# Optimization experiments

Measured on AMD Instinct MI355X. Metric: run time of the kernel, lower is better.

Reference implementation:

```python
import jax, jax.numpy as jnp
import numpy as np

B, T, D = 4, 2048, 1024
EPS = 1e-5


def _layernorm(x, g, b):
    mu = jnp.mean(x, axis=-1, keepdims=True)
    var = jnp.var(x, axis=-1, keepdims=True)
    return (x - mu) * jax.lax.rsqrt(var + EPS) * g + b


def setup_inputs() -> dict:
    key = jax.random.key(0)
    ks = jax.random.split(key, 16)
    s = lambda fan_in: 1.0 / np.sqrt(fan_in)
    return {
        "x": jax.random.normal(ks[0], (B, T, D), dtype=jnp.float32),
        "ln1_g": jnp.ones((D,), jnp.float32),
        "ln1_b": jnp.zeros((D,), jnp.float32),
        "Wqkv": jax.random.uniform(ks[1], (D, 3 * D), jnp.float32, -s(D), s(D)),
        "bqkv": jnp.zeros((3 * D,), jnp.float32),
        "Wproj": jax.random.uniform(ks[2], (D, D), jnp.float32, -s(D), s(D)),
        "bproj": jnp.zeros((D,), jnp.float32),
        "ln2_g": jnp.ones((D,), jnp.float32),
        "ln2_b": jnp.zeros((D,), jnp.float32),
        "W1": jax.random.uniform(ks[3], (D, 4 * D), jnp.float32, -s(D), s(D)),
        "b1": jnp.zeros((4 * D,), jnp.float32),
        "W2": jax.random.uniform(ks[4], (4 * D, D), jnp.float32, -s(4 * D), s(4 * D)),
        "b2": jnp.zeros((D,), jnp.float32),
    }


def reference(x, ln1_g, ln1_b, Wqkv, bqkv, Wproj, bproj, ln2_g, ln2_b, W1, b1, W2, b2):
    # NOTE: no residual connections in the original Block.
    h = _layernorm(x, ln1_g, ln1_b)
    kqv = h @ Wqkv + bqkv                      # [B,T,3D]
    k, q, v = jnp.split(kqv, 3, axis=-1)       # split order: k, q, v
    # Original scales by 1/sqrt(k.size(-1)) AFTER transposing k -> 1/sqrt(T).
    scores = jnp.einsum("btd,bsd->bts", q, k) * (1.0 / np.sqrt(T))
    causal = jnp.tril(jnp.ones((T, T), dtype=bool))
    scores = jnp.where(causal, scores, -jnp.inf)
    attn = jax.nn.softmax(scores, axis=-1)
    a = jnp.einsum("bts,bsd->btd", attn, v)
    a = a @ Wproj + bproj
    h2 = _layernorm(a, ln2_g, ln2_b)
    m = jax.nn.gelu(h2 @ W1 + b1, approximate=True)
    return m @ W2 + b2
```

## Files before the change

kernel.cpp:

```cpp
#include <hip/hip_runtime.h>
#include <hip/hip_bf16.h>

typedef __hip_bfloat16 bf16;
typedef __bf16 bf16x8 __attribute__((ext_vector_type(8)));
typedef __bf16 bf16x4 __attribute__((ext_vector_type(4)));
typedef __bf16 bf16x2 __attribute__((ext_vector_type(2)));
typedef float f32x4 __attribute__((ext_vector_type(4)));

static constexpr int Bq = 4, Tq = 2048, Dq = 1024;

__device__ inline float b2f(bf16 h) { return __bfloat162float(h); }
__device__ inline bf16 f2b(float f) { return __float2bfloat16(f); }

__device__ __forceinline__ void gload_lds16(const bf16* g, bf16* lds_wave_base) {
    __builtin_amdgcn_global_load_lds((const __attribute__((address_space(1))) void*)g,
                                     (__attribute__((address_space(3))) void*)lds_wave_base,
                                     16, 0, 0);
}

__device__ __forceinline__ float fast_gelu(float x) {
    float u = x * (0.7978845608028654f + 0.03567740814183427f * x * x);
    float e = __builtin_amdgcn_exp2f(-2.885390081777927f * u);
    return x * __builtin_amdgcn_rcpf(1.f + e);
}

__device__ inline void ld4f(const float* p, float* v) {
    float4 t = *reinterpret_cast<const float4*>(p);
    v[0] = t.x; v[1] = t.y; v[2] = t.z; v[3] = t.w;
}
__device__ inline void ld4f(const bf16* p, float* v) {
    bf16x4 t = *reinterpret_cast<const bf16x4*>(p);
    v[0] = (float)t[0]; v[1] = (float)t[1]; v[2] = (float)t[2]; v[3] = (float)t[3];
}

template <typename Tin>
__device__ __forceinline__ void ln_body(const Tin* __restrict__ x, const float* __restrict__ g,
                                        const float* __restrict__ b, bf16* __restrict__ out,
                                        int row, float* sred)
{
    const int tid = threadIdx.x;
    const int s0 = tid * 4;
    const Tin* xr = x + (size_t)row * Dq;
    bf16* orow = out + (size_t)row * Dq;
    float v[4], gv[4], bv[4];
    ld4f(xr + s0, v);
    ld4f(g + s0, gv);
    ld4f(b + s0, bv);
    float sum = v[0] + v[1] + v[2] + v[3];
    float sq = v[0]*v[0] + v[1]*v[1] + v[2]*v[2] + v[3]*v[3];
    for (int o = 32; o > 0; o >>= 1) { sum += __shfl_xor(sum, o); sq += __shfl_xor(sq, o); }
    const int w = tid >> 6;
    if ((tid & 63) == 0) { sred[w] = sum; sred[4 + w] = sq; }
    __syncthreads();
    const float ts = sred[0] + sred[1] + sred[2] + sred[3];
    const float tq = sred[4] + sred[5] + sred[6] + sred[7];
    const float mean = ts / Dq;
    const float rs = rsqrtf(tq / Dq - mean * mean + 1e-5f);
    bf16x4 o4;
    #pragma unroll
    for (int i = 0; i < 4; ++i) o4[i] = (__bf16)((v[i] - mean) * rs * gv[i] + bv[i]);
    *reinterpret_cast<bf16x4*>(orow + s0) = o4;
}

__global__ void ln_kernel(const bf16* __restrict__ x, const float* __restrict__ g,
                          const float* __restrict__ b, bf16* __restrict__ out)
{
    __shared__ float sred[8];
    ln_body(x, g, b, out, blockIdx.x, sred);
}

__global__ void prep_kernel(const float* __restrict__ x, const float* __restrict__ g,
                            const float* __restrict__ b, bf16* __restrict__ h,
                            const float* __restrict__ Wqkv, bf16* __restrict__ WqkvT,
                            const float* __restrict__ Wproj, bf16* __restrict__ WprojT,
                            const float* __restrict__ W1, bf16* __restrict__ W1T,
                            const float* __restrict__ W2, bf16* __restrict__ W2T)
{
    __shared__ float smem[64 * 65];
    int id = blockIdx.x;
    if (id < 8192) { ln_body(x, g, b, h, id, smem); return; }
    id -= 8192;
    const float* src; bf16* dst; long ldin, ldout; int gx;
    if (id < 768)       { src = Wqkv;  dst = WqkvT;  ldin = 3072; ldout = 1024; gx = 48; }
    else if (id < 1024) { id -= 768;  src = Wproj; dst = WprojT; ldin = 1024; ldout = 1024; gx = 16; }
    else if (id < 2048) { id -= 1024; src = W1;    dst = W1T;    ldin = 4096; ldout = 1024; gx = 64; }
    else                { id -= 2048; src = W2;    dst = W2T;    ldin = 1024; ldout = 4096; gx = 16; }
    const int c0 = (id % gx) * 64, r0 = (id / gx) * 64;
    const int tid = threadIdx.x;
    const int tx = tid & 63, ty = tid >> 6;
    float (*tile)[65] = reinterpret_cast<float(*)[65]>(smem);
    #pragma unroll
    for (int i = 0; i < 16; ++i) {
        int r = ty + i * 4;
        tile[r][tx] = src[(size_t)(r0 + r) * ldin + c0 + tx];
    }
    __syncthreads();
    const int px = tid & 31, cy = tid >> 5;
    #pragma unroll
    for (int i = 0; i < 8; ++i) {
        int cc = cy + i * 8;
        bf16x2 p;
        p[0] = (__bf16)tile[px * 2][cc];
        p[1] = (__bf16)tile[px * 2 + 1][cc];
        *reinterpret_cast<bf16x2*>(&dst[(size_t)(c0 + cc) * ldout + r0 + px * 2]) = p;
    }
}

__global__ void transpose_b2b_kernel(const bf16* __restrict__ in, bf16* __restrict__ out,
                                     long ldin, long ldout, long inBatch, long outBatch)
{
    __shared__ bf16 tile[64][66];
    const bf16* ip = in + (size_t)blockIdx.z * inBatch;
    bf16* op = out + (size_t)blockIdx.z * outBatch;
    const int c0 = blockIdx.x * 64, r0 = blockIdx.y * 64;
    const int tid = threadIdx.x;
    const int tx = tid & 31, ty = tid >> 5;
    #pragma unroll
    for (int i = 0; i < 8; ++i) {
        int r = ty + i * 8;
        *reinterpret_cast<bf16x2*>(&tile[r][tx * 2]) =
            *reinterpret_cast<const bf16x2*>(&ip[(size_t)(r0 + r) * ldin + c0 + tx * 2]);
    }
    __syncthreads();
    #pragma unroll
    for (int i = 0; i < 8; ++i) {
        int cc = ty + i * 8;
        bf16x2 p;
        p[0] = tile[tx * 2][cc];
        p[1] = tile[tx * 2 + 1][cc];
        *reinterpret_cast<bf16x2*>(&op[(size_t)(c0 + cc) * ldout + r0 + tx * 2]) = p;
    }
}

template <int ACT, int TRI, int CK, int FR>
__global__ void gemm128(const bf16* __restrict__ A, const bf16* __restrict__ Bt,
                        const float* __restrict__ bias,
                        bf16* __restrict__ Cb, float* __restrict__ Cf,
                        int K, long lda, long ldb, long ldc,
                        long sA, long sB, long sC, float scale)
{
    int bx, by;
    if (TRI) {
        const int lin = blockIdx.x;
        int t = (int)((sqrtf(8.f * lin + 1.f) - 1.f) * 0.5f);
        while ((t + 1) * (t + 2) / 2 <= lin) ++t;
        while (t * (t + 1) / 2 > lin) --t;
        by = t; bx = lin - t * (t + 1) / 2;
    } else {
        const int gx = gridDim.x, gy = gridDim.y;
        const int lin = blockIdx.x + gx * blockIdx.y;
        const int band = lin & 7;
        const int idx = lin >> 3;
        bx = idx % gx;
        by = band * (gy >> 3) + idx / gx;
    }

    const int m0 = by * 128, n0 = bx * 128;
    const int Kend = CK ? min(K, m0 + 128) : K;

    __shared__ bf16 As[128 * 64];
    __shared__ bf16 Bs[128 * 64];

    const bf16* Ab = A + (size_t)blockIdx.z * sA;
    const bf16* Bb = Bt + (size_t)blockIdx.z * sB;
    const int tid = threadIdx.x;
    const int wid = tid >> 6, lane = tid & 63;
    const int wr = wid >> 1, wc = wid & 1;
    const int l15 = lane & 15, quad = lane >> 4;

    const int rloc = lane >> 3, slot = lane & 7;
    const bf16* agp = Ab + (size_t)(m0 + wid * 32 + rloc) * lda + (slot ^ rloc) * 8;
    const bf16* bgp = Bb + (size_t)(n0 + wid * 32 + rloc) * ldb + (slot ^ rloc) * 8;
    bf16* awb = As + wid * 32 * 64;
    bf16* bwb = Bs + wid * 32 * 64;

    const int afo = (wr * 64 + l15) * 64 + ((quad ^ (l15 & 7)) * 8);
    const int bfo = (wc * 64 + l15) * 64 + ((quad ^ (l15 & 7)) * 8);

    f32x4 acc[4][4];
    #pragma unroll
    for (int i = 0; i < 4; ++i)
        #pragma unroll
        for (int j = 0; j < 4; ++j) acc[i][j] = (f32x4){0.f, 0.f, 0.f, 0.f};

    f32x4 acc_l[4];
    bf16x8 ones;
    if (FR) {
        #pragma unroll
        for (int i = 0; i < 4; ++i) acc_l[i] = (f32x4){0.f, 0.f, 0.f, 0.f};
        #pragma unroll
        for (int i = 0; i < 8; ++i) ones[i] = (__bf16)1.0f;
    }

    for (int k0 = 0; k0 < Kend; k0 += 64) {
        #pragma unroll
        for (int i = 0; i < 4; ++i) {
            gload_lds16(agp + k0 + (size_t)(i * 8) * lda, awb + i * 8 * 64);
            gload_lds16(bgp + k0 + (size_t)(i * 8) * ldb, bwb + i * 8 * 64);
        }
        __syncthreads();

        bf16x8 af0[4], bf0[4], af1[4], bf1[4];
        #pragma unroll
        for (int i = 0; i < 4; ++i) {
            af0[i] = *reinterpret_cast<const bf16x8*>(As + (afo ^ 0)  + i * 1024);
            af1[i] = *reinterpret_cast<const bf16x8*>(As + (afo ^ 32) + i * 1024);
        }
        #pragma unroll
        for (int j = 0; j < 4; ++j) {
            bf0[j] = *reinterpret_cast<const bf16x8*>(Bs + (bfo ^ 0)  + j * 1024);
            bf1[j] = *reinterpret_cast<const bf16x8*>(Bs + (bfo ^ 32) + j * 1024);
        }
        #pragma unroll
        for (int i = 0; i < 4; ++i)
            #pragma unroll
            for (int j = 0; j < 4; ++j)
                acc[i][j] = __builtin_amdgcn_mfma_f32_16x16x32_bf16(af0[i], bf0[j], acc[i][j], 0, 0, 0);
        if (FR) {
            #pragma unroll
            for (int i = 0; i < 4; ++i)
                acc_l[i] = __builtin_amdgcn_mfma_f32_16x16x32_bf16(af0[i], ones, acc_l[i], 0, 0, 0);
        }
        #pragma unroll
        for (int i = 0; i < 4; ++i)
            #pragma unroll
            for (int j = 0; j < 4; ++j)
                acc[i][j] = __builtin_amdgcn_mfma_f32_16x16x32_bf16(af1[i], bf1[j], acc[i][j], 0, 0, 0);
        if (FR) {
            #pragma unroll
            for (int i = 0; i < 4; ++i)
                acc_l[i] = __builtin_amdgcn_mfma_f32_16x16x32_bf16(af1[i], ones, acc_l[i], 0, 0, 0);
        }

        __syncthreads();
    }

    #pragma unroll
    for (int i = 0; i < 4; ++i) {
        const int row = m0 + wr * 64 + i * 16 + quad * 4;
        #pragma unroll
        for (int j = 0; j < 4; ++j) {
            const int col = n0 + wc * 64 + j * 16 + l15;
            const float bv = bias ? bias[col] : 0.f;
            #pragma unroll
            for (int r = 0; r < 4; ++r) {
                float vv = scale * acc[i][j][r] + bv;
                if (ACT == 1) vv = fast_gelu(vv);
                else if (ACT == 2)
                    vv = (col <= row + r) ? __builtin_amdgcn_exp2f(1.4426950408889634f * vv) : 0.f;
                if (FR) vv *= __builtin_amdgcn_rcpf(acc_l[i][r]);
                const size_t idx2 = (size_t)(row + r) * ldc + col + (size_t)blockIdx.z * sC;
                if (Cf) Cf[idx2] = vv;
                else    Cb[idx2] = f2b(vv);
            }
        }
    }
}

extern "C" void kernel_launch(void* const* d_in, const int* in_sizes, int n_in,
                              void* d_out, int out_size, void* d_ws, size_t ws_size,
                              hipStream_t stream)
{
    (void)in_sizes; (void)n_in; (void)out_size; (void)ws_size;
    const float* x     = (const float*)d_in[0];
    const float* ln1g  = (const float*)d_in[1];
    const float* ln1b  = (const float*)d_in[2];
    const float* Wqkv  = (const float*)d_in[3];
    const float* bqkv  = (const float*)d_in[4];
    const float* Wproj = (const float*)d_in[5];
    const float* bproj = (const float*)d_in[6];
    const float* ln2g  = (const float*)d_in[7];
    const float* ln2b  = (const float*)d_in[8];
    const float* W1    = (const float*)d_in[9];
    const float* b1    = (const float*)d_in[10];
    const float* W2    = (const float*)d_in[11];
    const float* b2    = (const float*)d_in[12];
    float* out = (float*)d_out;

    char* ws = (char*)d_ws;
    size_t off = 0;
    auto alloc = [&](size_t elems) { bf16* p = (bf16*)(ws + off); off += elems * sizeof(bf16); return p; };
    bf16* WqkvT  = alloc(3072UL * 1024);
    bf16* WprojT = alloc(1024UL * 1024);
    bf16* W1T    = alloc(4096UL * 1024);
    bf16* W2T    = alloc(1024UL * 4096);
    bf16* h      = alloc(8192UL * 1024);
    bf16* kqv    = alloc(8192UL * 3072);
    bf16* vT     = alloc(4UL * 1024 * 2048);
    bf16* attn   = alloc(4UL * 2048 * 2048);
    bf16* a   = h;
    bf16* p   = kqv;
    bf16* h2  = kqv + 8192UL * 1024;
    bf16* m   = kqv + 2UL * 8192 * 1024;

    const long T3D = (long)Tq * 3072, TT = (long)Tq * Tq, DT = (long)Dq * Tq, TD = (long)Tq * Dq;

    prep_kernel<<<11264, 256, 0, stream>>>(x, ln1g, ln1b, h,
                                           Wqkv, WqkvT, Wproj, WprojT, W1, W1T, W2, W2T);

    gemm128<0,0,0,0><<<dim3(24, 64, 1), 256, 0, stream>>>(h, WqkvT, bqkv, kqv, nullptr,
        1024, 1024L, 1024L, 3072L, 0L, 0L, 0L, 1.f);

    transpose_b2b_kernel<<<dim3(16, 32, 4), 256, 0, stream>>>(kqv + 2048, vT, 3072L, 2048L, T3D, DT);

    gemm128<2,1,0,0><<<dim3(136, 1, 4), 256, 0, stream>>>(kqv + 1024, kqv, nullptr, attn, nullptr,
        1024, 3072L, 3072L, 2048L, T3D, T3D, TT, 0.022097086912079608f);

    gemm128<0,0,1,1><<<dim3(8, 16, 4), 256, 0, stream>>>(attn, vT, nullptr, a, nullptr,
        2048, 2048L, 2048L, 1024L, TT, DT, TD, 1.f);

    gemm128<0,0,0,0><<<dim3(8, 64, 1), 256, 0, stream>>>(a, WprojT, bproj, p, nullptr,
        1024, 1024L, 1024L, 1024L, 0L, 0L, 0L, 1.f);

    ln_kernel<<<8192, 256, 0, stream>>>(p, ln2g, ln2b, h2);

    gemm128<1,0,0,0><<<dim3(32, 64, 1), 256, 0, stream>>>(h2, W1T, b1, m, nullptr,
        1024, 1024L, 1024L, 4096L, 0L, 0L, 0L, 1.f);

    gemm128<0,0,0,0><<<dim3(8, 64, 1), 256, 0, stream>>>(m, W2T, b2, nullptr, out,
        4096, 4096L, 4096L, 1024L, 0L, 0L, 0L, 1.f);
}
```

Before: 499.6 us.

## Switch GEMM to 32x32x16 MFMA and fold V transpose into scores kernel

The GEMM inner loop moves from 16x16x32 MFMA tiles to 32x32x16 MFMA tiles, so each wave issues fewer, larger matrix instructions and keeps 2x2 f32x16 accumulators, with new LDS swizzled fragment addressing and a new epilogue row mapping. Separately, the V transpose kernel is removed and its work is done by extra blocks appended to the causal scores GEMM grid (blocks past 136), which saves one launch and lets the transpose overlap with the scores GEMM. The larger MFMA shape changes register pressure and LDS read patterns, and the fused grid mixes heterogeneous blocks in one launch.

```diff
diff --git a/kernel.cpp b/kernel.cpp
--- a/kernel.cpp
+++ b/kernel.cpp
@@ -6,6 +6,7 @@
 typedef __bf16 bf16x4 __attribute__((ext_vector_type(4)));
 typedef __bf16 bf16x2 __attribute__((ext_vector_type(2)));
 typedef float f32x4 __attribute__((ext_vector_type(4)));
+typedef float f32x16 __attribute__((ext_vector_type(16)));
 
 static constexpr int Bq = 4, Tq = 2048, Dq = 1024;
 
@@ -106,42 +107,45 @@
     }
 }
 
-__global__ void transpose_b2b_kernel(const bf16* __restrict__ in, bf16* __restrict__ out,
-                                     long ldin, long ldout, long inBatch, long outBatch)
-{
-    __shared__ bf16 tile[64][66];
-    const bf16* ip = in + (size_t)blockIdx.z * inBatch;
-    bf16* op = out + (size_t)blockIdx.z * outBatch;
-    const int c0 = blockIdx.x * 64, r0 = blockIdx.y * 64;
-    const int tid = threadIdx.x;
-    const int tx = tid & 31, ty = tid >> 5;
-    #pragma unroll
-    for (int i = 0; i < 8; ++i) {
-        int r = ty + i * 8;
-        *reinterpret_cast<bf16x2*>(&tile[r][tx * 2]) =
-            *reinterpret_cast<const bf16x2*>(&ip[(size_t)(r0 + r) * ldin + c0 + tx * 2]);
-    }
-    __syncthreads();
-    #pragma unroll
-    for (int i = 0; i < 8; ++i) {
-        int cc = ty + i * 8;
-        bf16x2 p;
-        p[0] = tile[tx * 2][cc];
-        p[1] = tile[tx * 2 + 1][cc];
-        *reinterpret_cast<bf16x2*>(&op[(size_t)(c0 + cc) * ldout + r0 + tx * 2]) = p;
-    }
-}
-
 template <int ACT, int TRI, int CK, int FR>
 __global__ void gemm128(const bf16* __restrict__ A, const bf16* __restrict__ Bt,
                         const float* __restrict__ bias,
                         bf16* __restrict__ Cb, float* __restrict__ Cf,
                         int K, long lda, long ldb, long ldc,
-                        long sA, long sB, long sC, float scale)
-{
+                        long sA, long sB, long sC, float scale,
+                        const bf16* __restrict__ vsrc, bf16* __restrict__ vdst)
+{
+    __shared__ bf16 As[128 * 64];
+    __shared__ bf16 Bs[128 * 64];
+
     int bx, by;
     if (TRI) {
         const int lin = blockIdx.x;
+        if (lin >= 136) {
+            const int idx = lin - 136;
+            const int c0 = (idx & 15) * 64, r0 = (idx >> 4) * 64;
+            const bf16* ip = vsrc + (size_t)blockIdx.z * ((size_t)Tq * 3072);
+            bf16* op = vdst + (size_t)blockIdx.z * ((size_t)Dq * Tq);
+            bf16 (*tile)[66] = reinterpret_cast<bf16(*)[66]>(As);
+            const int tid = threadIdx.x;
+            const int tx = tid & 31, ty = tid >> 5;
+            #pragma unroll
+            for (int i = 0; i < 8; ++i) {
+                int r = ty + i * 8;
+                *reinterpret_cast<bf16x2*>(&tile[r][tx * 2]) =
+                    *reinterpret_cast<const bf16x2*>(&ip[(size_t)(r0 + r) * 3072 + c0 + tx * 2]);
+            }
+            __syncthreads();
+            #pragma unroll
+            for (int i = 0; i < 8; ++i) {
+                int cc = ty + i * 8;
+                bf16x2 p;
+                p[0] = tile[tx * 2][cc];
+                p[1] = tile[tx * 2 + 1][cc];
+                *reinterpret_cast<bf16x2*>(&op[(size_t)(c0 + cc) * 2048 + r0 + tx * 2]) = p;
+            }
+            return;
+        }
         int t = (int)((sqrtf(8.f * lin + 1.f) - 1.f) * 0.5f);
         while ((t + 1) * (t + 2) / 2 <= lin) ++t;
         while (t * (t + 1) / 2 > lin) --t;
@@ -158,15 +162,12 @@
     const int m0 = by * 128, n0 = bx * 128;
     const int Kend = CK ? min(K, m0 + 128) : K;
 
-    __shared__ bf16 As[128 * 64];
-    __shared__ bf16 Bs[128 * 64];
-
     const bf16* Ab = A + (size_t)blockIdx.z * sA;
     const bf16* Bb = Bt + (size_t)blockIdx.z * sB;
     const int tid = threadIdx.x;
     const int wid = tid >> 6, lane = tid & 63;
     const int wr = wid >> 1, wc = wid & 1;
-    const int l15 = lane & 15, quad = lane >> 4;
+    const int l31 = lane & 31, khalf = lane >> 5, l7 = lane & 7;
 
     const int rloc = lane >> 3, slot = lane & 7;
     const bf16* agp = Ab + (size_t)(m0 + wid * 32 + rloc) * lda + (slot ^ rloc) * 8;
@@ -174,20 +175,24 @@
     bf16* awb = As + wid * 32 * 64;
     bf16* bwb = Bs + wid * 32 * 64;
 
-    const int afo = (wr * 64 + l15) * 64 + ((quad ^ (l15 & 7)) * 8);
-    const int bfo = (wc * 64 + l15) * 64 + ((quad ^ (l15 & 7)) * 8);
-
-    f32x4 acc[4][4];
-    #pragma unroll
-    for (int i = 0; i < 4; ++i)
-        #pragma unroll
-        for (int j = 0; j < 4; ++j) acc[i][j] = (f32x4){0.f, 0.f, 0.f, 0.f};
-
-    f32x4 acc_l[4];
+    const int rowA0 = (wr * 64 + l31) * 64, rowA1 = rowA0 + 32 * 64;
+    const int rowB0 = (wc * 64 + l31) * 64, rowB1 = rowB0 + 32 * 64;
+
+    f32x16 acc[2][2];
+    #pragma unroll
+    for (int i = 0; i < 2; ++i)
+        #pragma unroll
+        for (int j = 0; j < 2; ++j)
+            #pragma unroll
+            for (int r = 0; r < 16; ++r) acc[i][j][r] = 0.f;
+
+    f32x16 acc_l[2];
     bf16x8 ones;
     if (FR) {
         #pragma unroll
-        for (int i = 0; i < 4; ++i) acc_l[i] = (f32x4){0.f, 0.f, 0.f, 0.f};
+        for (int i = 0; i < 2; ++i)
+            #pragma unroll
+            for (int r = 0; r < 16; ++r) acc_l[i][r] = 0.f;
         #pragma unroll
         for (int i = 0; i < 8; ++i) ones[i] = (__bf16)1.0f;
     }
@@ -200,58 +205,54 @@
         }
         __syncthreads();
 
-        bf16x8 af0[4], bf0[4], af1[4], bf1[4];
-        #pragma unroll
-        for (int i = 0; i < 4; ++i) {
-            af0[i] = *reinterpret_cast<const bf16x8*>(As + (afo ^ 0)  + i * 1024);
-            af1[i] = *reinterpret_cast<const bf16x8*>(As + (afo ^ 32) + i * 1024);
-        }
-        #pragma unroll
-        for (int j = 0; j < 4; ++j) {
-            bf0[j] = *reinterpret_cast<const bf16x8*>(Bs + (bfo ^ 0)  + j * 1024);
-            bf1[j] = *reinterpret_cast<const bf16x8*>(Bs + (bfo ^ 32) + j * 1024);
-        }
-        #pragma unroll
-        for (int i = 0; i < 4; ++i)
-            #pragma unroll
-            for (int j = 0; j < 4; ++j)
-                acc[i][j] = __builtin_amdgcn_mfma_f32_16x16x32_bf16(af0[i], bf0[j], acc[i][j], 0, 0, 0);
-        if (FR) {
-            #pragma unroll
-            for (int i = 0; i < 4; ++i)
-                acc_l[i] = __builtin_amdgcn_mfma_f32_16x16x32_bf16(af0[i], ones, acc_l[i], 0, 0, 0);
-        }
-        #pragma unroll
-        for (int i = 0; i < 4; ++i)
-            #pragma unroll
-            for (int j = 0; j < 4; ++j)
-                acc[i][j] = __builtin_amdgcn_mfma_f32_16x16x32_bf16(af1[i], bf1[j], acc[i][j], 0, 0, 0);
-        if (FR) {
-            #pragma unroll
-            for (int i = 0; i < 4; ++i)
-                acc_l[i] = __builtin_amdgcn_mfma_f32_16x16x32_bf16(af1[i], ones, acc_l[i], 0, 0, 0);
+        bf16x8 af[2][4], bff[2][4];
+        #pragma unroll
+        for (int c = 0; c < 4; ++c) {
+            const int sx = ((c * 2 + khalf) ^ l7) * 8;
+            af[0][c]  = *reinterpret_cast<const bf16x8*>(As + rowA0 + sx);
+            af[1][c]  = *reinterpret_cast<const bf16x8*>(As + rowA1 + sx);
+            bff[0][c] = *reinterpret_cast<const bf16x8*>(Bs + rowB0 + sx);
+            bff[1][c] = *reinterpret_cast<const bf16x8*>(Bs + rowB1 + sx);
+        }
+        #pragma unroll
+        for (int c = 0; c < 4; ++c) {
+            #pragma unroll
+            for (int i = 0; i < 2; ++i)
+                #pragma unroll
+                for (int j = 0; j < 2; ++j)
+                    acc[i][j] = __builtin_amdgcn_mfma_f32_32x32x16_bf16(af[i][c], bff[j][c], acc[i][j], 0, 0, 0);
+            if (FR) {
+                #pragma unroll
+                for (int i = 0; i < 2; ++i)
+                    acc_l[i] = __builtin_amdgcn_mfma_f32_32x32x16_bf16(af[i][c], ones, acc_l[i], 0, 0, 0);
+            }
         }
 
         __syncthreads();
     }
 
     #pragma unroll
-    for (int i = 0; i < 4; ++i) {
-        const int row = m0 + wr * 64 + i * 16 + quad * 4;
-        #pragma unroll
-        for (int j = 0; j < 4; ++j) {
-            const int col = n0 + wc * 64 + j * 16 + l15;
+    for (int i = 0; i < 2; ++i) {
+        const int rbase = m0 + wr * 64 + i * 32 + 4 * khalf;
+        #pragma unroll
+        for (int j = 0; j < 2; ++j) {
+            const int col = n0 + wc * 64 + j * 32 + l31;
             const float bv = bias ? bias[col] : 0.f;
             #pragma unroll
-            for (int r = 0; r < 4; ++r) {
-                float vv = scale * acc[i][j][r] + bv;
-                if (ACT == 1) vv = fast_gelu(vv);
-                else if (ACT == 2)
-                    vv = (col <= row + r) ? __builtin_amdgcn_exp2f(1.4426950408889634f * vv) : 0.f;
-                if (FR) vv *= __builtin_amdgcn_rcpf(acc_l[i][r]);
-                const size_t idx2 = (size_t)(row + r) * ldc + col + (size_t)blockIdx.z * sC;
-                if (Cf) Cf[idx2] = vv;
-                else    Cb[idx2] = f2b(vv);
+            for (int q = 0; q < 4; ++q) {
+                #pragma unroll
+                for (int r = 0; r < 4; ++r) {
+                    const int reg = q * 4 + r;
+                    const int row = rbase + 8 * q + r;
+                    float vv = scale * acc[i][j][reg] + bv;
+                    if (ACT == 1) vv = fast_gelu(vv);
+                    else if (ACT == 2)
+                        vv = (col <= row) ? __builtin_amdgcn_exp2f(1.4426950408889634f * vv) : 0.f;
+                    if (FR) vv *= __builtin_amdgcn_rcpf(acc_l[i][reg]);
+                    const size_t idx2 = (size_t)row * ldc + col + (size_t)blockIdx.z * sC;
+                    if (Cf) Cf[idx2] = vv;
+                    else    Cb[idx2] = f2b(vv);
+                }
             }
         }
     }
@@ -299,24 +300,22 @@
                                            Wqkv, WqkvT, Wproj, WprojT, W1, W1T, W2, W2T);
 
     gemm128<0,0,0,0><<<dim3(24, 64, 1), 256, 0, stream>>>(h, WqkvT, bqkv, kqv, nullptr,
-        1024, 1024L, 1024L, 3072L, 0L, 0L, 0L, 1.f);
-
-    transpose_b2b_kernel<<<dim3(16, 32, 4), 256, 0, stream>>>(kqv + 2048, vT, 3072L, 2048L, T3D, DT);
-
-    gemm128<2,1,0,0><<<dim3(136, 1, 4), 256, 0, stream>>>(kqv + 1024, kqv, nullptr, attn, nullptr,
-        1024, 3072L, 3072L, 2048L, T3D, T3D, TT, 0.022097086912079608f);
+        1024, 1024L, 1024L, 3072L, 0L, 0L, 0L, 1.f, nullptr, nullptr);
+
+    gemm128<2,1,0,0><<<dim3(648, 1, 4), 256, 0, stream>>>(kqv + 1024, kqv, nullptr, attn, nullptr,
+        1024, 3072L, 3072L, 2048L, T3D, T3D, TT, 0.022097086912079608f, kqv + 2048, vT);
 
     gemm128<0,0,1,1><<<dim3(8, 16, 4), 256, 0, stream>>>(attn, vT, nullptr, a, nullptr,
-        2048, 2048L, 2048L, 1024L, TT, DT, TD, 1.f);
+        2048, 2048L, 2048L, 1024L, TT, DT, TD, 1.f, nullptr, nullptr);
 
     gemm128<0,0,0,0><<<dim3(8, 64, 1), 256, 0, stream>>>(a, WprojT, bproj, p, nullptr,
-        1024, 1024L, 1024L, 1024L, 0L, 0L, 0L, 1.f);
+        1024, 1024L, 1024L, 1024L, 0L, 0L, 0L, 1.f, nullptr, nullptr);
 
     ln_kernel<<<8192, 256, 0, stream>>>(p, ln2g, ln2b, h2);
 
     gemm128<1,0,0,0><<<dim3(32, 64, 1), 256, 0, stream>>>(h2, W1T, b1, m, nullptr,
-        1024, 1024L, 1024L, 4096L, 0L, 0L, 0L, 1.f);
+        1024, 1024L, 1024L, 4096L, 0L, 0L, 0L, 1.f, nullptr, nullptr);
 
     gemm128<0,0,0,0><<<dim3(8, 64, 1), 256, 0, stream>>>(m, W2T, b2, nullptr, out,
-        4096, 4096L, 4096L, 1024L, 0L, 0L, 0L, 1.f);
-}
+        4096, 4096L, 4096L, 1024L, 0L, 0L, 0L, 1.f, nullptr, nullptr);
+}
```

Result: slower. 539.5 us (+8.0%).

## Fuse post-prep stages into persistent megakernel with software grid barriers

Applied to the files above, without the earlier changes.

Replaces the eight separate GEMM, transpose and layernorm launches with one persistent kernel of 768 blocks. The blocks loop over the tiles of each stage and meet at an atomic-counter grid barrier between stages. The V transpose now runs in the same phase as the causal QK^T GEMM. This is meant to remove launch gaps and kernel tail effects. In exchange it caps parallelism at 768 co-resident blocks, leaves idle blocks in the 512-tile phases, and relies on all blocks being resident at once, or the spin barrier can deadlock.

```diff
diff --git a/kernel.cpp b/kernel.cpp
--- a/kernel.cpp
+++ b/kernel.cpp
@@ -8,6 +8,7 @@
 typedef float f32x4 __attribute__((ext_vector_type(4)));
 
 static constexpr int Bq = 4, Tq = 2048, Dq = 1024;
+static constexpr int NBLK = 768;
 
 __device__ inline float b2f(bf16 h) { return __bfloat162float(h); }
 __device__ inline bf16 f2b(float f) { return __float2bfloat16(f); }
@@ -31,6 +32,24 @@
 __device__ inline void ld4f(const bf16* p, float* v) {
     bf16x4 t = *reinterpret_cast<const bf16x4*>(p);
     v[0] = (float)t[0]; v[1] = (float)t[1]; v[2] = (float)t[2]; v[3] = (float)t[3];
+}
+
+__device__ __forceinline__ void grid_sync(unsigned* bar) {
+    __syncthreads();
+    if (threadIdx.x == 0) {
+        __threadfence();
+        unsigned g = __hip_atomic_load(bar + 1, __ATOMIC_RELAXED, __HIP_MEMORY_SCOPE_AGENT);
+        unsigned a = __hip_atomic_fetch_add(bar, 1u, __ATOMIC_ACQ_REL, __HIP_MEMORY_SCOPE_AGENT);
+        if (a == NBLK - 1u) {
+            __hip_atomic_store(bar, 0u, __ATOMIC_RELAXED, __HIP_MEMORY_SCOPE_AGENT);
+            __hip_atomic_fetch_add(bar + 1, 1u, __ATOMIC_RELEASE, __HIP_MEMORY_SCOPE_AGENT);
+        } else {
+            while (__hip_atomic_load(bar + 1, __ATOMIC_ACQUIRE, __HIP_MEMORY_SCOPE_AGENT) == g)
+                __builtin_amdgcn_s_sleep(2);
+        }
+        __threadfence();
+    }
+    __syncthreads();
 }
 
 template <typename Tin>
@@ -62,22 +81,20 @@
     *reinterpret_cast<bf16x4*>(orow + s0) = o4;
 }
 
-__global__ void ln_kernel(const bf16* __restrict__ x, const float* __restrict__ g,
-                          const float* __restrict__ b, bf16* __restrict__ out)
-{
-    __shared__ float sred[8];
-    ln_body(x, g, b, out, blockIdx.x, sred);
-}
-
 __global__ void prep_kernel(const float* __restrict__ x, const float* __restrict__ g,
                             const float* __restrict__ b, bf16* __restrict__ h,
                             const float* __restrict__ Wqkv, bf16* __restrict__ WqkvT,
                             const float* __restrict__ Wproj, bf16* __restrict__ WprojT,
                             const float* __restrict__ W1, bf16* __restrict__ W1T,
-                            const float* __restrict__ W2, bf16* __restrict__ W2T)
+                            const float* __restrict__ W2, bf16* __restrict__ W2T,
+                            unsigned* __restrict__ bar)
 {
     __shared__ float smem[64 * 65];
     int id = blockIdx.x;
+    if (id == 0 && threadIdx.x == 0) {
+        __hip_atomic_store(bar, 0u, __ATOMIC_RELAXED, __HIP_MEMORY_SCOPE_AGENT);
+        __hip_atomic_store(bar + 1, 0u, __ATOMIC_RELAXED, __HIP_MEMORY_SCOPE_AGENT);
+    }
     if (id < 8192) { ln_body(x, g, b, h, id, smem); return; }
     id -= 8192;
     const float* src; bf16* dst; long ldin, ldout; int gx;
@@ -106,71 +123,29 @@
     }
 }
 
-__global__ void transpose_b2b_kernel(const bf16* __restrict__ in, bf16* __restrict__ out,
-                                     long ldin, long ldout, long inBatch, long outBatch)
-{
-    __shared__ bf16 tile[64][66];
-    const bf16* ip = in + (size_t)blockIdx.z * inBatch;
-    bf16* op = out + (size_t)blockIdx.z * outBatch;
-    const int c0 = blockIdx.x * 64, r0 = blockIdx.y * 64;
-    const int tid = threadIdx.x;
-    const int tx = tid & 31, ty = tid >> 5;
-    #pragma unroll
-    for (int i = 0; i < 8; ++i) {
-        int r = ty + i * 8;
-        *reinterpret_cast<bf16x2*>(&tile[r][tx * 2]) =
-            *reinterpret_cast<const bf16x2*>(&ip[(size_t)(r0 + r) * ldin + c0 + tx * 2]);
-    }
-    __syncthreads();
-    #pragma unroll
-    for (int i = 0; i < 8; ++i) {
-        int cc = ty + i * 8;
-        bf16x2 p;
-        p[0] = tile[tx * 2][cc];
-        p[1] = tile[tx * 2 + 1][cc];
-        *reinterpret_cast<bf16x2*>(&op[(size_t)(c0 + cc) * ldout + r0 + tx * 2]) = p;
-    }
-}
-
-template <int ACT, int TRI, int CK, int FR>
-__global__ void gemm128(const bf16* __restrict__ A, const bf16* __restrict__ Bt,
-                        const float* __restrict__ bias,
-                        bf16* __restrict__ Cb, float* __restrict__ Cf,
-                        int K, long lda, long ldb, long ldc,
-                        long sA, long sB, long sC, float scale)
-{
-    int bx, by;
-    if (TRI) {
-        const int lin = blockIdx.x;
-        int t = (int)((sqrtf(8.f * lin + 1.f) - 1.f) * 0.5f);
-        while ((t + 1) * (t + 2) / 2 <= lin) ++t;
-        while (t * (t + 1) / 2 > lin) --t;
-        by = t; bx = lin - t * (t + 1) / 2;
-    } else {
-        const int gx = gridDim.x, gy = gridDim.y;
-        const int lin = blockIdx.x + gx * blockIdx.y;
-        const int band = lin & 7;
-        const int idx = lin >> 3;
-        bx = idx % gx;
-        by = band * (gy >> 3) + idx / gx;
-    }
-
-    const int m0 = by * 128, n0 = bx * 128;
+__device__ __forceinline__ void band_remap(int lin, int gx, int gy, int& bx, int& by) {
+    const int band = lin & 7;
+    const int idx = lin >> 3;
+    bx = idx % gx;
+    by = band * (gy >> 3) + idx / gx;
+}
+
+template <int ACT, int CK, int FR>
+__device__ __forceinline__ void gemm_tile(const bf16* __restrict__ A, const bf16* __restrict__ Bt,
+                                          const float* __restrict__ bias,
+                                          bf16* __restrict__ Cb, float* __restrict__ Cf,
+                                          int K, long lda, long ldb, long ldc, float scale,
+                                          int m0, int n0, bf16* As, bf16* Bs)
+{
     const int Kend = CK ? min(K, m0 + 128) : K;
-
-    __shared__ bf16 As[128 * 64];
-    __shared__ bf16 Bs[128 * 64];
-
-    const bf16* Ab = A + (size_t)blockIdx.z * sA;
-    const bf16* Bb = Bt + (size_t)blockIdx.z * sB;
     const int tid = threadIdx.x;
     const int wid = tid >> 6, lane = tid & 63;
     const int wr = wid >> 1, wc = wid & 1;
     const int l15 = lane & 15, quad = lane >> 4;
 
     const int rloc = lane >> 3, slot = lane & 7;
-    const bf16* agp = Ab + (size_t)(m0 + wid * 32 + rloc) * lda + (slot ^ rloc) * 8;
-    const bf16* bgp = Bb + (size_t)(n0 + wid * 32 + rloc) * ldb + (slot ^ rloc) * 8;
+    const bf16* agp = A + (size_t)(m0 + wid * 32 + rloc) * lda + (slot ^ rloc) * 8;
+    const bf16* bgp = Bt + (size_t)(n0 + wid * 32 + rloc) * ldb + (slot ^ rloc) * 8;
     bf16* awb = As + wid * 32 * 64;
     bf16* bwb = Bs + wid * 32 * 64;
 
@@ -249,11 +224,113 @@
                 else if (ACT == 2)
                     vv = (col <= row + r) ? __builtin_amdgcn_exp2f(1.4426950408889634f * vv) : 0.f;
                 if (FR) vv *= __builtin_amdgcn_rcpf(acc_l[i][r]);
-                const size_t idx2 = (size_t)(row + r) * ldc + col + (size_t)blockIdx.z * sC;
+                const size_t idx2 = (size_t)(row + r) * ldc + col;
                 if (Cf) Cf[idx2] = vv;
                 else    Cb[idx2] = f2b(vv);
             }
         }
+    }
+}
+
+__device__ __forceinline__ void vtrans_tile(const bf16* __restrict__ ip, bf16* __restrict__ op,
+                                            int idx, bf16* smem)
+{
+    __syncthreads();
+    bf16 (*tile)[66] = reinterpret_cast<bf16(*)[66]>(smem);
+    const int c0 = (idx & 15) * 64, r0 = (idx >> 4) * 64;
+    const int tid = threadIdx.x;
+    const int tx = tid & 31, ty = tid >> 5;
+    #pragma unroll
+    for (int i = 0; i < 8; ++i) {
+        int r = ty + i * 8;
+        *reinterpret_cast<bf16x2*>(&tile[r][tx * 2]) =
+            *reinterpret_cast<const bf16x2*>(&ip[(size_t)(r0 + r) * 3072 + c0 + tx * 2]);
+    }
+    __syncthreads();
+    #pragma unroll
+    for (int i = 0; i < 8; ++i) {
+        int cc = ty + i * 8;
+        bf16x2 p;
+        p[0] = tile[tx * 2][cc];
+        p[1] = tile[tx * 2 + 1][cc];
+        *reinterpret_cast<bf16x2*>(&op[(size_t)(c0 + cc) * 2048 + r0 + tx * 2]) = p;
+    }
+    __syncthreads();
+}
+
+__global__ __launch_bounds__(256, 3)
+void mega_kernel(const bf16* __restrict__ h, bf16* __restrict__ kqv, bf16* __restrict__ vT,
+                 bf16* __restrict__ attn, bf16* __restrict__ a, bf16* __restrict__ p,
+                 bf16* __restrict__ h2, bf16* __restrict__ m, float* __restrict__ out,
+                 const bf16* __restrict__ WqkvT, const float* __restrict__ bqkv,
+                 const bf16* __restrict__ WprojT, const float* __restrict__ bproj,
+                 const float* __restrict__ ln2g, const float* __restrict__ ln2b,
+                 const bf16* __restrict__ W1T, const float* __restrict__ b1,
+                 const bf16* __restrict__ W2T, const float* __restrict__ b2,
+                 unsigned* __restrict__ bar)
+{
+    __shared__ bf16 As[128 * 64];
+    __shared__ bf16 Bs[128 * 64];
+    const int blk = blockIdx.x;
+    const long T3D = (long)Tq * 3072, TT = (long)Tq * Tq, DT = (long)Dq * Tq, TD = (long)Tq * Dq;
+
+    for (int t = blk; t < 1536; t += NBLK) {
+        int bx, by; band_remap(t, 24, 64, bx, by);
+        gemm_tile<0,0,0>(h, WqkvT, bqkv, kqv, nullptr, 1024, 1024L, 1024L, 3072L, 1.f,
+                         by * 128, bx * 128, As, Bs);
+    }
+    grid_sync(bar);
+
+    for (int t = blk; t < 2592; t += NBLK) {
+        if (t < 544) {
+            const int z = t / 136, lin = t % 136;
+            int by = (int)((sqrtf(8.f * lin + 1.f) - 1.f) * 0.5f);
+            while ((by + 1) * (by + 2) / 2 <= lin) ++by;
+            while (by * (by + 1) / 2 > lin) --by;
+            const int bx = lin - by * (by + 1) / 2;
+            gemm_tile<2,0,0>(kqv + 1024 + (size_t)z * T3D, kqv + (size_t)z * T3D, nullptr,
+                             attn + (size_t)z * TT, nullptr, 1024, 3072L, 3072L, 2048L,
+                             0.022097086912079608f, by * 128, bx * 128, As, Bs);
+        } else {
+            const int j = t - 544, z = j >> 9, idx = j & 511;
+            vtrans_tile(kqv + 2048 + (size_t)z * T3D, vT + (size_t)z * DT, idx, As);
+        }
+    }
+    grid_sync(bar);
+
+    if (blk < 512) {
+        const int z = blk >> 7, lin = blk & 127;
+        int bx, by; band_remap(lin, 8, 16, bx, by);
+        gemm_tile<0,1,1>(attn + (size_t)z * TT, vT + (size_t)z * DT, nullptr,
+                         a + (size_t)z * TD, nullptr, 2048, 2048L, 2048L, 1024L, 1.f,
+                         by * 128, bx * 128, As, Bs);
+    }
+    grid_sync(bar);
+
+    if (blk < 512) {
+        int bx, by; band_remap(blk, 8, 64, bx, by);
+        gemm_tile<0,0,0>(a, WprojT, bproj, p, nullptr, 1024, 1024L, 1024L, 1024L, 1.f,
+                         by * 128, bx * 128, As, Bs);
+    }
+    grid_sync(bar);
+
+    for (int r = blk; r < 8192; r += NBLK) {
+        ln_body(p, ln2g, ln2b, h2, r, reinterpret_cast<float*>(As));
+        __syncthreads();
+    }
+    grid_sync(bar);
+
+    for (int t = blk; t < 2048; t += NBLK) {
+        int bx, by; band_remap(t, 32, 64, bx, by);
+        gemm_tile<1,0,0>(h2, W1T, b1, m, nullptr, 1024, 1024L, 1024L, 4096L, 1.f,
+                         by * 128, bx * 128, As, Bs);
+    }
+    grid_sync(bar);
+
+    if (blk < 512) {
+        int bx, by; band_remap(blk, 8, 64, bx, by);
+        gemm_tile<0,0,0>(m, W2T, b2, nullptr, out, 4096, 4096L, 4096L, 1024L, 1.f,
+                         by * 128, bx * 128, As, Bs);
     }
 }
 
@@ -288,35 +365,16 @@
     bf16* kqv    = alloc(8192UL * 3072);
     bf16* vT     = alloc(4UL * 1024 * 2048);
     bf16* attn   = alloc(4UL * 2048 * 2048);
+    unsigned* bar = (unsigned*)alloc(64);
     bf16* a   = h;
     bf16* p   = kqv;
     bf16* h2  = kqv + 8192UL * 1024;
     bf16* m   = kqv + 2UL * 8192 * 1024;
 
-    const long T3D = (long)Tq * 3072, TT = (long)Tq * Tq, DT = (long)Dq * Tq, TD = (long)Tq * Dq;
-
     prep_kernel<<<11264, 256, 0, stream>>>(x, ln1g, ln1b, h,
-                                           Wqkv, WqkvT, Wproj, WprojT, W1, W1T, W2, W2T);
-
-    gemm128<0,0,0,0><<<dim3(24, 64, 1), 256, 0, stream>>>(h, WqkvT, bqkv, kqv, nullptr,
-        1024, 1024L, 1024L, 3072L, 0L, 0L, 0L, 1.f);
-
-    transpose_b2b_kernel<<<dim3(16, 32, 4), 256, 0, stream>>>(kqv + 2048, vT, 3072L, 2048L, T3D, DT);
-
-    gemm128<2,1,0,0><<<dim3(136, 1, 4), 256, 0, stream>>>(kqv + 1024, kqv, nullptr, attn, nullptr,
-        1024, 3072L, 3072L, 2048L, T3D, T3D, TT, 0.022097086912079608f);
-
-    gemm128<0,0,1,1><<<dim3(8, 16, 4), 256, 0, stream>>>(attn, vT, nullptr, a, nullptr,
-        2048, 2048L, 2048L, 1024L, TT, DT, TD, 1.f);
-
-    gemm128<0,0,0,0><<<dim3(8, 64, 1), 256, 0, stream>>>(a, WprojT, bproj, p, nullptr,
-        1024, 1024L, 1024L, 1024L, 0L, 0L, 0L, 1.f);
-
-    ln_kernel<<<8192, 256, 0, stream>>>(p, ln2g, ln2b, h2);
-
-    gemm128<1,0,0,0><<<dim3(32, 64, 1), 256, 0, stream>>>(h2, W1T, b1, m, nullptr,
-        1024, 1024L, 1024L, 4096L, 0L, 0L, 0L, 1.f);
-
-    gemm128<0,0,0,0><<<dim3(8, 64, 1), 256, 0, stream>>>(m, W2T, b2, nullptr, out,
-        4096, 4096L, 4096L, 1024L, 0L, 0L, 0L, 1.f);
-}
+                                           Wqkv, WqkvT, Wproj, WprojT, W1, W1T, W2, W2T, bar);
+
+    mega_kernel<<<NBLK, 256, 0, stream>>>(h, kqv, vT, attn, a, p, h2, m, out,
+                                          WqkvT, bqkv, WprojT, bproj, ln2g, ln2b,
+                                          W1T, b1, W2T, b2, bar);
+}
```

Measured after the change: 1.614 ms. 223% more time.
